# Kernel tuning notes

Hardware: AMD Instinct MI355X
Metric: run time of the kernel (lower is better)

Reference implementation:

```python
import jax, jax.numpy as jnp
import numpy as np

EPS_AREA = 1e-6   # guard against zero box area in the OKS-style feedback
EPS_BCE = 1e-7    # clamp probabilities for binary cross entropy


def setup_inputs() -> dict:
    key = jax.random.key(0)
    k0, k1, k2, k3, k4 = jax.random.split(key, 5)
    L, Lp, K = 512, 64, 17
    pred_poses = jax.random.uniform(k0, (L, K, 3), dtype=jnp.float32)
    target_poses = jax.random.uniform(k1, (Lp, K, 3), dtype=jnp.float32)
    pred_feedbacks = jax.random.uniform(k2, (L,), dtype=jnp.float32)
    ious = jax.random.uniform(k3, (L, Lp), dtype=jnp.float32)
    target_areas = jax.random.uniform(k4, (Lp,), dtype=jnp.float32)
    return {
        "pred_poses": pred_poses,
        "target_poses": target_poses,
        "pred_feedbacks": pred_feedbacks,
        "ious": ious,
        "target_areas": target_areas,
        "features_dim": 56,
    }


def reference(pred_poses, target_poses, pred_feedbacks, ious, target_areas, features_dim):
    L, K, _ = pred_poses.shape
    Lp = target_poses.shape[0]

    # ---- preprocess_poses: [L, K, 3] -> [L, 3K, D, D] ----
    # Original loops over keypoints emitting torch.full maps in (x, y, v) order per
    # keypoint, which is exactly a reshape to [L, 3K] followed by spatial broadcast.
    features_poses = jnp.broadcast_to(
        pred_poses.reshape(L, 3 * K, 1, 1),
        (L, 3 * K, features_dim, features_dim),
    )

    # ---- compute_loss (interpolate_poses=False branch), fully vectorized ----
    pred_xy = pred_poses[:, :, :2]     # [L, K, 2]
    targ_xy = target_poses[:, :, :2]   # [Lp, K, 2]
    # pairwise squared keypoint distances: [L, Lp, K]
    d2 = jnp.sum((pred_xy[:, None] - targ_xy[None]) ** 2, axis=-1)
    # OKS-style target feedback per (pred, target) pair: [L, Lp]
    targ_feedback = jnp.mean(
        jnp.exp(-d2 / (2.0 * target_areas[None, :, None] + EPS_AREA)), axis=-1
    )
    # MSE feedback loss per pair
    feedback_loss = (pred_feedbacks[:, None] - targ_feedback) ** 2  # [L, Lp]

    # binary cross entropy on visibility channel, mean over K per pair
    pv = jnp.clip(pred_poses[:, :, 2], EPS_BCE, 1.0 - EPS_BCE)  # [L, K]
    tv = target_poses[:, :, 2]                                   # [Lp, K]
    bce = -(tv[None] * jnp.log(pv[:, None]) + (1.0 - tv[None]) * jnp.log(1.0 - pv[:, None]))
    bce = jnp.mean(bce, axis=-1)  # [L, Lp]

    loss = jnp.sum(ious * (feedback_loss + bce))
    return features_poses, loss
```

## Files before the change

### kernel.cpp

```cpp
#include <hip/hip_runtime.h>
#include <math.h>

#define EPS_AREA 1e-6f
#define EPS_BCE  1e-7f

typedef float v4f __attribute__((ext_vector_type(4)));

__global__ __launch_bounds__(256) void broadcast_kernel(
    const float* __restrict__ pred, float* __restrict__ out,
    int rows, long inner, int inner4)
{
    const int wave = threadIdx.x >> 6;
    const int lane = threadIdx.x & 63;
    const int row  = blockIdx.x * 4 + wave;
    if (row >= rows) return;

    const float v = pred[row];
    v4f val;
    val.x = v; val.y = v; val.z = v; val.w = v;

    float* rowp = out + (size_t)row * (size_t)inner;
    v4f* dst = (v4f*)rowp;
    for (int i = lane; i < inner4; i += 64)
        dst[i] = val;

    const int rem = (int)(inner - (long)inner4 * 4);
    if (rem && lane < rem)
        rowp[(size_t)inner4 * 4 + lane] = v;
}

__global__ __launch_bounds__(64) void loss_partial_kernel(
    const float* __restrict__ pred_poses,
    const float* __restrict__ target_poses,
    const float* __restrict__ pred_feedbacks,
    const float* __restrict__ ious,
    const float* __restrict__ target_areas,
    float* __restrict__ partial,
    int Lp, int K)
{
    extern __shared__ float sm[];
    float* px  = sm;
    float* py  = sm + K;
    float* lpv = sm + 2 * K;
    float* l1m = sm + 3 * K;

    const int l   = blockIdx.x;
    const int tid = threadIdx.x;

    if (tid < K) {
        const float* p = pred_poses + ((size_t)l * K + tid) * 3;
        px[tid] = p[0];
        py[tid] = p[1];
        float pv = fminf(fmaxf(p[2], EPS_BCE), 1.0f - EPS_BCE);
        lpv[tid] = logf(pv);
        l1m[tid] = logf(1.0f - pv);
    }
    __syncthreads();

    float acc = 0.0f;
    for (int lp = tid; lp < Lp; lp += 64) {
        const float  invDen = 1.0f / (2.0f * target_areas[lp] + EPS_AREA);
        const float* t = target_poses + (size_t)lp * K * 3;
        float sumExp = 0.0f;
        float sBce   = 0.0f;
        for (int k = 0; k < K; ++k) {
            float tx = t[3 * k + 0];
            float ty = t[3 * k + 1];
            float tv = t[3 * k + 2];
            float dx = px[k] - tx;
            float dy = py[k] - ty;
            float d2 = dx * dx + dy * dy;
            sumExp += expf(-d2 * invDen);
            sBce   += tv * lpv[k] + (1.0f - tv) * l1m[k];
        }
        float tf  = sumExp / (float)K;
        float d   = pred_feedbacks[l] - tf;
        acc += ious[(size_t)l * Lp + lp] * (d * d - sBce / (float)K);
    }

    for (int off = 32; off > 0; off >>= 1)
        acc += __shfl_down(acc, off, 64);
    if (tid == 0)
        partial[l] = acc;
}

__global__ __launch_bounds__(256) void loss_reduce_kernel(
    const float* __restrict__ partial, float* __restrict__ loss_out, int L)
{
    __shared__ float wsum[4];
    float s = 0.0f;
    for (int i = threadIdx.x; i < L; i += 256)
        s += partial[i];
    for (int off = 32; off > 0; off >>= 1)
        s += __shfl_down(s, off, 64);
    const int wave = threadIdx.x >> 6;
    const int lane = threadIdx.x & 63;
    if (lane == 0) wsum[wave] = s;
    __syncthreads();
    if (threadIdx.x == 0)
        *loss_out = wsum[0] + wsum[1] + wsum[2] + wsum[3];
}

extern "C" void kernel_launch(void* const* d_in, const int* in_sizes, int n_in,
                              void* d_out, int out_size, void* d_ws, size_t ws_size,
                              hipStream_t stream) {
    const float* pred_poses     = (const float*)d_in[0];
    const float* target_poses   = (const float*)d_in[1];
    const float* pred_feedbacks = (const float*)d_in[2];
    const float* ious           = (const float*)d_in[3];
    const float* target_areas   = (const float*)d_in[4];
    float* out = (float*)d_out;

    const int L  = in_sizes[2];
    const int Lp = in_sizes[4];
    const int K  = in_sizes[0] / (3 * L);

    const long rows  = (long)L * 3 * K;
    const long inner = ((long)out_size - 1) / rows;
    const int  inner4 = (int)(inner / 4);

    float* loss_slot = out + ((size_t)out_size - 1);
    float* partial   = (float*)d_ws;

    broadcast_kernel<<<(int)((rows + 3) / 4), 256, 0, stream>>>(
        pred_poses, out, (int)rows, inner, inner4);

    const size_t smem = 4 * (size_t)K * sizeof(float);
    loss_partial_kernel<<<L, 64, smem, stream>>>(
        pred_poses, target_poses, pred_feedbacks, ious, target_areas,
        partial, Lp, K);

    loss_reduce_kernel<<<1, 256, 0, stream>>>(partial, loss_slot, L);
}
```

Measured before the change: 347.3 us.

## Flatten broadcast with constant row width, fuse final reduction, parallelize loss over K

Replaces the per-row broadcast with a grid-stride flat vector store kernel specialized for a row width of 784 float4s, and moves the final loss reduction into it to remove one launch. The loss partial kernel now uses four waves per block that split keypoints, then reduce through shared memory, and it uses fast exp. It also reorders the loss kernel before the broadcast. Fast exp may change accuracy slightly, and the per-element integer division adds index cost.

```diff
diff --git a/kernel.cpp b/kernel.cpp
--- a/kernel.cpp
+++ b/kernel.cpp
@@ -6,7 +6,32 @@
 
 typedef float v4f __attribute__((ext_vector_type(4)));
 
-__global__ __launch_bounds__(256) void broadcast_kernel(
+template <int INNER4>
+__global__ __launch_bounds__(256) void broadcast_flat_kernel(
+    const float* __restrict__ pred, float* __restrict__ out,
+    unsigned int total4,
+    const float* __restrict__ partial, float* __restrict__ loss_out, int L)
+{
+    if (blockIdx.x == 0 && threadIdx.x < 64) {
+        float s = 0.0f;
+        for (int i = threadIdx.x; i < L; i += 64) s += partial[i];
+        for (int off = 32; off > 0; off >>= 1) s += __shfl_down(s, off, 64);
+        if (threadIdx.x == 0) *loss_out = s;
+    }
+
+    v4f* dst = (v4f*)out;
+    const unsigned int stride = gridDim.x * blockDim.x;
+    for (unsigned int i = blockIdx.x * blockDim.x + threadIdx.x; i < total4;
+         i += stride) {
+        const unsigned int row = i / (unsigned int)INNER4;
+        const float v = pred[row];
+        v4f val;
+        val.x = v; val.y = v; val.z = v; val.w = v;
+        dst[i] = val;
+    }
+}
+
+__global__ __launch_bounds__(256) void broadcast_rows_kernel(
     const float* __restrict__ pred, float* __restrict__ out,
     int rows, long inner, int inner4)
 {
@@ -14,22 +39,17 @@
     const int lane = threadIdx.x & 63;
     const int row  = blockIdx.x * 4 + wave;
     if (row >= rows) return;
-
     const float v = pred[row];
     v4f val;
     val.x = v; val.y = v; val.z = v; val.w = v;
-
     float* rowp = out + (size_t)row * (size_t)inner;
     v4f* dst = (v4f*)rowp;
-    for (int i = lane; i < inner4; i += 64)
-        dst[i] = val;
-
+    for (int i = lane; i < inner4; i += 64) dst[i] = val;
     const int rem = (int)(inner - (long)inner4 * 4);
-    if (rem && lane < rem)
-        rowp[(size_t)inner4 * 4 + lane] = v;
-}
-
-__global__ __launch_bounds__(64) void loss_partial_kernel(
+    if (rem && lane < rem) rowp[(size_t)inner4 * 4 + lane] = v;
+}
+
+__global__ __launch_bounds__(256) void loss_partial4_kernel(
     const float* __restrict__ pred_poses,
     const float* __restrict__ target_poses,
     const float* __restrict__ pred_feedbacks,
@@ -43,9 +63,12 @@
     float* py  = sm + K;
     float* lpv = sm + 2 * K;
     float* l1m = sm + 3 * K;
-
-    const int l   = blockIdx.x;
-    const int tid = threadIdx.x;
+    float* red = sm + 4 * K;
+
+    const int l    = blockIdx.x;
+    const int tid  = threadIdx.x;
+    const int w    = tid >> 6;
+    const int lane = tid & 63;
 
     if (tid < K) {
         const float* p = pred_poses + ((size_t)l * K + tid) * 3;
@@ -57,31 +80,80 @@
     }
     __syncthreads();
 
-    float acc = 0.0f;
-    for (int lp = tid; lp < Lp; lp += 64) {
-        const float  invDen = 1.0f / (2.0f * target_areas[lp] + EPS_AREA);
-        const float* t = target_poses + (size_t)lp * K * 3;
-        float sumExp = 0.0f;
-        float sBce   = 0.0f;
-        for (int k = 0; k < K; ++k) {
+    float eS = 0.0f, bS = 0.0f;
+    if (lane < Lp) {
+        const float  invDen = 1.0f / (2.0f * target_areas[lane] + EPS_AREA);
+        const float* t = target_poses + (size_t)lane * K * 3;
+        for (int k = w; k < K; k += 4) {
             float tx = t[3 * k + 0];
             float ty = t[3 * k + 1];
             float tv = t[3 * k + 2];
             float dx = px[k] - tx;
             float dy = py[k] - ty;
             float d2 = dx * dx + dy * dy;
-            sumExp += expf(-d2 * invDen);
-            sBce   += tv * lpv[k] + (1.0f - tv) * l1m[k];
+            eS += __expf(-d2 * invDen);
+            bS += fmaf(tv, lpv[k] - l1m[k], l1m[k]);
         }
-        float tf  = sumExp / (float)K;
-        float d   = pred_feedbacks[l] - tf;
-        acc += ious[(size_t)l * Lp + lp] * (d * d - sBce / (float)K);
-    }
-
-    for (int off = 32; off > 0; off >>= 1)
-        acc += __shfl_down(acc, off, 64);
-    if (tid == 0)
-        partial[l] = acc;
+    }
+    red[tid]       = eS;
+    red[256 + tid] = bS;
+    __syncthreads();
+
+    if (w == 0) {
+        float eSum = red[lane] + red[64 + lane] + red[128 + lane] + red[192 + lane];
+        float bSum = red[256 + lane] + red[320 + lane] + red[384 + lane] + red[448 + lane];
+        float val = 0.0f;
+        if (lane < Lp) {
+            float tf = eSum / (float)K;
+            float d  = pred_feedbacks[l] - tf;
+            val = ious[(size_t)l * Lp + lane] * (d * d - bSum / (float)K);
+        }
+        for (int off = 32; off > 0; off >>= 1) val += __shfl_down(val, off, 64);
+        if (lane == 0) partial[l] = val;
+    }
+}
+
+__global__ __launch_bounds__(64) void loss_partial1_kernel(
+    const float* __restrict__ pred_poses, const float* __restrict__ target_poses,
+    const float* __restrict__ pred_feedbacks, const float* __restrict__ ious,
+    const float* __restrict__ target_areas, float* __restrict__ partial,
+    int Lp, int K)
+{
+    extern __shared__ float sm[];
+    float* px  = sm;
+    float* py  = sm + K;
+    float* lpv = sm + 2 * K;
+    float* l1m = sm + 3 * K;
+
+    const int l   = blockIdx.x;
+    const int tid = threadIdx.x;
+    if (tid < K) {
+        const float* p = pred_poses + ((size_t)l * K + tid) * 3;
+        px[tid] = p[0];
+        py[tid] = p[1];
+        float pv = fminf(fmaxf(p[2], EPS_BCE), 1.0f - EPS_BCE);
+        lpv[tid] = logf(pv);
+        l1m[tid] = logf(1.0f - pv);
+    }
+    __syncthreads();
+
+    float acc = 0.0f;
+    for (int lp = tid; lp < Lp; lp += 64) {
+        const float  invDen = 1.0f / (2.0f * target_areas[lp] + EPS_AREA);
+        const float* t = target_poses + (size_t)lp * K * 3;
+        float eS = 0.0f, bS = 0.0f;
+        for (int k = 0; k < K; ++k) {
+            float dx = px[k] - t[3 * k + 0];
+            float dy = py[k] - t[3 * k + 1];
+            float tv = t[3 * k + 2];
+            eS += __expf(-(dx * dx + dy * dy) * invDen);
+            bS += fmaf(tv, lpv[k] - l1m[k], l1m[k]);
+        }
+        float d = pred_feedbacks[l] - eS / (float)K;
+        acc += ious[(size_t)l * Lp + lp] * (d * d - bS / (float)K);
+    }
+    for (int off = 32; off > 0; off >>= 1) acc += __shfl_down(acc, off, 64);
+    if (tid == 0) partial[l] = acc;
 }
 
 __global__ __launch_bounds__(256) void loss_reduce_kernel(
@@ -89,16 +161,11 @@
 {
     __shared__ float wsum[4];
     float s = 0.0f;
-    for (int i = threadIdx.x; i < L; i += 256)
-        s += partial[i];
-    for (int off = 32; off > 0; off >>= 1)
-        s += __shfl_down(s, off, 64);
-    const int wave = threadIdx.x >> 6;
-    const int lane = threadIdx.x & 63;
-    if (lane == 0) wsum[wave] = s;
-    __syncthreads();
-    if (threadIdx.x == 0)
-        *loss_out = wsum[0] + wsum[1] + wsum[2] + wsum[3];
+    for (int i = threadIdx.x; i < L; i += 256) s += partial[i];
+    for (int off = 32; off > 0; off >>= 1) s += __shfl_down(s, off, 64);
+    if ((threadIdx.x & 63) == 0) wsum[threadIdx.x >> 6] = s;
+    __syncthreads();
+    if (threadIdx.x == 0) *loss_out = wsum[0] + wsum[1] + wsum[2] + wsum[3];
 }
 
 extern "C" void kernel_launch(void* const* d_in, const int* in_sizes, int n_in,
@@ -115,20 +182,33 @@
     const int Lp = in_sizes[4];
     const int K  = in_sizes[0] / (3 * L);
 
-    const long rows  = (long)L * 3 * K;
-    const long inner = ((long)out_size - 1) / rows;
+    const long rows   = (long)L * 3 * K;
+    const long inner  = ((long)out_size - 1) / rows;
     const int  inner4 = (int)(inner / 4);
+    const int  rem    = (int)(inner - (long)inner4 * 4);
 
     float* loss_slot = out + ((size_t)out_size - 1);
     float* partial   = (float*)d_ws;
 
-    broadcast_kernel<<<(int)((rows + 3) / 4), 256, 0, stream>>>(
-        pred_poses, out, (int)rows, inner, inner4);
-
-    const size_t smem = 4 * (size_t)K * sizeof(float);
-    loss_partial_kernel<<<L, 64, smem, stream>>>(
-        pred_poses, target_poses, pred_feedbacks, ious, target_areas,
-        partial, Lp, K);
-
-    loss_reduce_kernel<<<1, 256, 0, stream>>>(partial, loss_slot, L);
-}
+    if (Lp <= 64) {
+        const size_t smem = (4 * (size_t)K + 512) * sizeof(float);
+        loss_partial4_kernel<<<L, 256, smem, stream>>>(
+            pred_poses, target_poses, pred_feedbacks, ious, target_areas,
+            partial, Lp, K);
+    } else {
+        const size_t smem = 4 * (size_t)K * sizeof(float);
+        loss_partial1_kernel<<<L, 64, smem, stream>>>(
+            pred_poses, target_poses, pred_feedbacks, ious, target_areas,
+            partial, Lp, K);
+    }
+
+    if (inner4 == 784 && rem == 0) {
+        const unsigned int total4 = (unsigned int)(rows * 784);
+        broadcast_flat_kernel<784><<<4096, 256, 0, stream>>>(
+            pred_poses, out, total4, partial, loss_slot, L);
+    } else {
+        broadcast_rows_kernel<<<(int)((rows + 3) / 4), 256, 0, stream>>>(
+            pred_poses, out, (int)rows, inner, inner4);
+        loss_reduce_kernel<<<1, 256, 0, stream>>>(partial, loss_slot, L);
+    }
+}
```

New measurement: 335.9 us. 3.3% less time.
